# Kernel tuning notes

Measured on AMD Instinct MI355X. Metric: run time of the kernel, lower is better.

Reference implementation:

```python
import jax, jax.numpy as jnp
import numpy as np

DIM = 256
HEADS = 8
DIM_HEAD = 64
INNER = HEADS * DIM_HEAD  # 512
B, N = 4, 1024


def setup_inputs() -> dict:
    key = jax.random.key(0)
    ks = jax.random.split(key, 7)
    x = jax.random.normal(ks[0], (B, N, DIM), dtype=jnp.float32)
    attn_bias = jax.random.normal(ks[1], (B, HEADS, N, N), dtype=jnp.float32)
    s = 1.0 / np.sqrt(DIM)
    Wq = jax.random.normal(ks[2], (DIM, INNER), dtype=jnp.float32) * s
    Wkv = jax.random.normal(ks[3], (DIM, 2 * INNER), dtype=jnp.float32) * s
    # to_out initialized to zero in the torch module; use small random so output is non-trivial
    Wo = jax.random.normal(ks[4], (INNER, DIM), dtype=jnp.float32) * (1.0 / np.sqrt(INNER))
    bo = jnp.zeros((DIM,), dtype=jnp.float32)
    # gating initialized weight=0, bias=1 -> sigmoid(1); use small random weight + bias 1
    Wg = jax.random.normal(ks[5], (DIM, INNER), dtype=jnp.float32) * 0.02
    bg = jnp.ones((INNER,), dtype=jnp.float32)
    return {"x": x, "attn_bias": attn_bias, "Wq": Wq, "Wkv": Wkv,
            "Wo": Wo, "bo": bo, "Wg": Wg, "bg": bg}


def reference(x, attn_bias, Wq, Wkv, Wo, bo, Wg, bg):
    b, n, _ = x.shape
    scale = DIM_HEAD ** -0.5
    q = x @ Wq                                    # [b, n, inner]
    kv = x @ Wkv                                  # [b, n, 2*inner]
    k, v = jnp.split(kv, 2, axis=-1)
    def split_heads(t):
        return t.reshape(b, n, HEADS, DIM_HEAD).transpose(0, 2, 1, 3)  # [b,h,n,d]
    q, k, v = split_heads(q) * scale, split_heads(k), split_heads(v)
    dots = jnp.einsum('bhid,bhjd->bhij', q, k) + attn_bias
    # explicit max-subtract then softmax (matches original; numerically identical)
    attn = jax.nn.softmax(dots, axis=-1)
    out = jnp.einsum('bhij,bhjd->bhid', attn, v)  # [b,h,n,d]
    out = out.transpose(0, 2, 1, 3).reshape(b, n, INNER)
    gates = jax.nn.sigmoid(x @ Wg + bg)
    out = out * gates
    return out @ Wo + bo
```

## Files before the change

### kernel.cpp

```cpp
#include <hip/hip_runtime.h>

typedef unsigned short u16;
typedef unsigned int u32;
typedef __attribute__((ext_vector_type(8))) __bf16 bf16x8;
typedef __attribute__((ext_vector_type(4))) float floatx4;
typedef const __attribute__((address_space(1))) unsigned char glob_u8;
typedef __attribute__((address_space(3))) unsigned char lds_u8;

#define DEV __device__ __forceinline__

DEV u16 f2bf(float f) {
  u32 u = __builtin_bit_cast(u32, f);
  u = (u + 0x7fffu + ((u >> 16) & 1u)) >> 16;
  return (u16)u;
}
DEV float bf2f(u16 h) {
  u32 u = ((u32)h) << 16;
  return __builtin_bit_cast(float, u);
}
DEV floatx4 MFMA(bf16x8 a, bf16x8 b, floatx4 c) {
  return __builtin_amdgcn_mfma_f32_16x16x32_bf16(a, b, c, 0, 0, 0);
}

__global__ void convert_k(const float* __restrict__ x, const float* __restrict__ Wq,
                          const float* __restrict__ Wkv, const float* __restrict__ Wg,
                          const float* __restrict__ Wo,
                          u16* __restrict__ xb, u16* __restrict__ WcatT, u16* __restrict__ WoT) {
  int i = blockIdx.x * 256 + threadIdx.x;
  if (i < 1048576) { xb[i] = f2bf(x[i]); return; }
  i -= 1048576;
  if (i < 524288) {
    int n = i >> 8, kk = i & 255;
    float v;
    if (n < 512) v = Wq[kk * 512 + n];
    else if (n < 1536) v = Wkv[kk * 1024 + (n - 512)];
    else v = Wg[kk * 512 + (n - 1536)];
    WcatT[i] = f2bf(v);
    return;
  }
  i -= 524288;
  if (i < 131072) {
    int n = i >> 9, kk = i & 511;
    WoT[i] = f2bf(Wo[kk * 256 + n]);
  }
}

__global__ __launch_bounds__(256, 4) void gemm_qkvg(
    const u16* __restrict__ xb, const u16* __restrict__ WcatT, const float* __restrict__ bg,
    u16* __restrict__ qb, u16* __restrict__ kfrag, u16* __restrict__ vfrag, u16* __restrict__ gb) {
  __shared__ __attribute__((aligned(16))) u16 As[128 * 40];
  __shared__ __attribute__((aligned(16))) u16 Bs[64 * 40];
  const int tid = threadIdx.x;
  const int wave = tid >> 6, lane = tid & 63;
  const int lane15 = lane & 15, quad = lane >> 4;
  const int rm0 = blockIdx.x * 128;
  const int cn0 = blockIdx.y * 64;
  const int wm = (wave & 1) * 64, wn = (wave >> 1) * 32;
  const int rowA = tid >> 1, segA = (tid & 1) * 16;
  const int rowB = tid >> 2, segB = (tid & 3) * 8;
  floatx4 acc[4][2] = {};
  uint4 a0 = *(const uint4*)(xb + (rm0 + rowA) * 256 + segA);
  uint4 a1 = *(const uint4*)(xb + (rm0 + rowA) * 256 + segA + 8);
  uint4 b0 = *(const uint4*)(WcatT + (cn0 + rowB) * 256 + segB);
#pragma unroll 1
  for (int k0 = 0; k0 < 256; k0 += 32) {
    __syncthreads();
    *(uint4*)(As + rowA * 40 + segA) = a0;
    *(uint4*)(As + rowA * 40 + segA + 8) = a1;
    *(uint4*)(Bs + rowB * 40 + segB) = b0;
    __syncthreads();
    if (k0 < 224) {
      a0 = *(const uint4*)(xb + (rm0 + rowA) * 256 + k0 + 32 + segA);
      a1 = *(const uint4*)(xb + (rm0 + rowA) * 256 + k0 + 32 + segA + 8);
      b0 = *(const uint4*)(WcatT + (cn0 + rowB) * 256 + k0 + 32 + segB);
    }
    bf16x8 af[4], bfr[2];
#pragma unroll
    for (int mt = 0; mt < 4; ++mt) af[mt] = *(const bf16x8*)(As + (wm + mt * 16 + lane15) * 40 + quad * 8);
#pragma unroll
    for (int nt = 0; nt < 2; ++nt) bfr[nt] = *(const bf16x8*)(Bs + (wn + nt * 16 + lane15) * 40 + quad * 8);
#pragma unroll
    for (int mt = 0; mt < 4; ++mt)
#pragma unroll
      for (int nt = 0; nt < 2; ++nt)
        acc[mt][nt] = MFMA(af[mt], bfr[nt], acc[mt][nt]);
  }
#pragma unroll
  for (int mt = 0; mt < 4; ++mt)
#pragma unroll
    for (int nt = 0; nt < 2; ++nt)
#pragma unroll
      for (int r = 0; r < 4; ++r) {
        int row = rm0 + wm + mt * 16 + quad * 4 + r;
        int col = cn0 + wn + nt * 16 + lane15;
        float v = acc[mt][nt][r];
        int b = row >> 10, n = row & 1023;
        if (col < 512) {
          int h = col >> 6, d = col & 63;
          qb[((b * 8 + h) * 1024 + n) * 64 + d] = f2bf(v * 0.125f);
        } else if (col < 1024) {
          int c = col - 512, h = c >> 6, d = c & 63;
          int bh2 = b * 8 + h;
          int t = n >> 4, l15 = n & 15;
          int half = d >> 5, qd = (d >> 3) & 3, e = d & 7;
          kfrag[(size_t)bh2 * 65536 + t * 1024 + half * 512 + (qd * 16 + l15) * 8 + e] = f2bf(v);
        } else if (col < 1536) {
          int c = col - 1024, h = c >> 6, d = c & 63;
          int bh2 = b * 8 + h;
          int t64 = n >> 6, ck = (n >> 5) & 1, qd = (n >> 3) & 3, e = n & 7;
          int dt = d >> 4, l15 = d & 15;
          vfrag[(size_t)bh2 * 65536 + t64 * 4096 + dt * 1024 + ck * 512 + (qd * 16 + l15) * 8 + e] = f2bf(v);
        } else {
          int c = col - 1536;
          float g = 1.0f / (1.0f + __expf(-(v + bg[c])));
          gb[row * 512 + c] = f2bf(g);
        }
      }
}

__global__ __launch_bounds__(256, 3) void attn_part_k(
    const u16* __restrict__ qb, const u16* __restrict__ kfrag, const u16* __restrict__ vfrag,
    const float* __restrict__ bias,
    float* __restrict__ po, float* __restrict__ pl) {
  __shared__ __attribute__((aligned(16))) u16 Kt[4096];
  __shared__ __attribute__((aligned(16))) u16 Vt[4096];
  __shared__ __attribute__((aligned(16))) float Bt[4096];
  __shared__ __attribute__((aligned(16))) u16 Ps[4 * 16 * 72];
  const int tid = threadIdx.x;
  const int wave = tid >> 6, lane = tid & 63;
  const int lane15 = lane & 15, quad = lane >> 4;
  const int bh = blockIdx.x;
  const int q0 = blockIdx.y * 64;
  const int kc = blockIdx.z;

  bf16x8 qf0, qf1;
  {
    const u16* qrow = qb + ((size_t)(bh * 1024 + q0 + wave * 16 + lane15)) * 64 + quad * 8;
    qf0 = *(const bf16x8*)(qrow);
    qf1 = *(const bf16x8*)(qrow + 32);
  }
  bf16x8 ones;
#pragma unroll
  for (int e = 0; e < 8; ++e) ones[e] = __builtin_bit_cast(__bf16, (u16)0x3F80);

  floatx4 oacc[4] = {};
  floatx4 lacc = {};

  u16* Pw = Ps + wave * (16 * 72);
  const u16* kp = kfrag + (size_t)bh * 65536;
  const u16* vp = vfrag + (size_t)bh * 65536;

#pragma unroll 1
  for (int kt = 0; kt < 8; ++kt) {
    const int kb0 = kc * 512 + kt * 64;
    const u16* kS = kp + kb0 * 64;
    const u16* vS = vp + kb0 * 64;
#pragma unroll
    for (int c = 0; c < 2; ++c) {
      int ch = wave * 2 + c;
      __builtin_amdgcn_global_load_lds((glob_u8*)(kS + ch * 512 + lane * 8),
                                       (lds_u8*)(Kt + ch * 512), 16, 0, 0);
      __builtin_amdgcn_global_load_lds((glob_u8*)(vS + ch * 512 + lane * 8),
                                       (lds_u8*)(Vt + ch * 512), 16, 0, 0);
    }
#pragma unroll
    for (int c = 0; c < 4; ++c) {
      int ch = wave * 4 + c;
      const float* bS = bias + ((size_t)(bh * 1024 + q0 + ch * 4 + (lane >> 4))) * 1024 + kb0 + (lane & 15) * 4;
      __builtin_amdgcn_global_load_lds((glob_u8*)bS, (lds_u8*)(Bt + ch * 256), 16, 0, 0);
    }
    __syncthreads();

    floatx4 s[4];
#pragma unroll
    for (int j = 0; j < 4; ++j) {
      bf16x8 kf0 = *(const bf16x8*)(Kt + j * 1024 + lane * 8);
      bf16x8 kf1 = *(const bf16x8*)(Kt + j * 1024 + 512 + lane * 8);
      floatx4 z = {};
      z = MFMA(qf0, kf0, z);
      s[j] = MFMA(qf1, kf1, z);
    }
#pragma unroll
    for (int j = 0; j < 4; ++j)
#pragma unroll
      for (int r = 0; r < 4; ++r)
        s[j][r] = __expf(s[j][r] + Bt[(wave * 16 + quad * 4 + r) * 64 + j * 16 + lane15] - 8.0f);
#pragma unroll
    for (int j = 0; j < 4; ++j)
#pragma unroll
      for (int r = 0; r < 4; ++r)
        Pw[(quad * 4 + r) * 72 + j * 16 + lane15] = f2bf(s[j][r]);
    bf16x8 pf0 = *(const bf16x8*)(Pw + lane15 * 72 + quad * 8);
    bf16x8 pf1 = *(const bf16x8*)(Pw + lane15 * 72 + 32 + quad * 8);

    lacc = MFMA(pf0, ones, lacc);
    lacc = MFMA(pf1, ones, lacc);
#pragma unroll
    for (int dt = 0; dt < 4; ++dt) {
      bf16x8 vf0 = *(const bf16x8*)(Vt + dt * 1024 + lane * 8);
      bf16x8 vf1 = *(const bf16x8*)(Vt + dt * 1024 + 512 + lane * 8);
      oacc[dt] = MFMA(pf0, vf0, oacc[dt]);
      oacc[dt] = MFMA(pf1, vf1, oacc[dt]);
    }
    __syncthreads();
  }

  float* poW = po + ((size_t)(kc * 32 + bh)) * 65536;
#pragma unroll
  for (int dt = 0; dt < 4; ++dt)
#pragma unroll
    for (int r = 0; r < 4; ++r) {
      int qrow = q0 + wave * 16 + quad * 4 + r;
      poW[(size_t)qrow * 64 + dt * 16 + lane15] = oacc[dt][r];
    }
  if (lane15 == 0) {
#pragma unroll
    for (int r = 0; r < 4; ++r) {
      int qrow = q0 + wave * 16 + quad * 4 + r;
      pl[kc * 32768 + bh * 1024 + qrow] = lacc[r];
    }
  }
}

__global__ __launch_bounds__(256) void attn_merge_k(
    const float* __restrict__ po, const float* __restrict__ pl,
    const u16* __restrict__ gb, u16* __restrict__ ogb) {
  int t = blockIdx.x * 256 + threadIdx.x;
  int row = t >> 4;
  int dseg = (t & 15) * 4;
  float inv = 1.0f / (pl[row] + pl[32768 + row]);
  float4 o0 = *(const float4*)(po + (size_t)row * 64 + dseg);
  float4 o1 = *(const float4*)(po + ((size_t)(32768 + row)) * 64 + dseg);
  int bh = row >> 10, q = row & 1023;
  int h = bh & 7, b = bh >> 3;
  size_t gi = ((size_t)(b * 1024 + q)) * 512 + h * 64 + dseg;
  u16 g4[4];
  *(uint2*)g4 = *(const uint2*)(gb + gi);
  u16 r4[4];
  r4[0] = f2bf((o0.x + o1.x) * inv * bf2f(g4[0]));
  r4[1] = f2bf((o0.y + o1.y) * inv * bf2f(g4[1]));
  r4[2] = f2bf((o0.z + o1.z) * inv * bf2f(g4[2]));
  r4[3] = f2bf((o0.w + o1.w) * inv * bf2f(g4[3]));
  *(uint2*)(ogb + gi) = *(uint2*)r4;
}

__global__ __launch_bounds__(256, 4) void gemm_out_part(
    const u16* __restrict__ og, const u16* __restrict__ WoT, float* __restrict__ pout) {
  __shared__ __attribute__((aligned(16))) u16 As[128 * 40];
  __shared__ __attribute__((aligned(16))) u16 Bs[64 * 40];
  const int tid = threadIdx.x;
  const int wave = tid >> 6, lane = tid & 63;
  const int lane15 = lane & 15, quad = lane >> 4;
  const int rm0 = blockIdx.x * 128;
  const int cn0 = blockIdx.y * 64;
  const int kc = blockIdx.z;
  const int wm = (wave & 1) * 64, wn = (wave >> 1) * 32;
  const int rowA = tid >> 1, segA = (tid & 1) * 16;
  const int rowB = tid >> 2, segB = (tid & 3) * 8;
  floatx4 acc[4][2] = {};
  uint4 a0 = *(const uint4*)(og + (rm0 + rowA) * 512 + kc * 128 + segA);
  uint4 a1 = *(const uint4*)(og + (rm0 + rowA) * 512 + kc * 128 + segA + 8);
  uint4 b0 = *(const uint4*)(WoT + (cn0 + rowB) * 512 + kc * 128 + segB);
#pragma unroll 1
  for (int s = 0; s < 4; ++s) {
    const int k0 = kc * 128 + s * 32;
    __syncthreads();
    *(uint4*)(As + rowA * 40 + segA) = a0;
    *(uint4*)(As + rowA * 40 + segA + 8) = a1;
    *(uint4*)(Bs + rowB * 40 + segB) = b0;
    __syncthreads();
    if (s < 3) {
      a0 = *(const uint4*)(og + (rm0 + rowA) * 512 + k0 + 32 + segA);
      a1 = *(const uint4*)(og + (rm0 + rowA) * 512 + k0 + 32 + segA + 8);
      b0 = *(const uint4*)(WoT + (cn0 + rowB) * 512 + k0 + 32 + segB);
    }
    bf16x8 af[4], bfr[2];
#pragma unroll
    for (int mt = 0; mt < 4; ++mt) af[mt] = *(const bf16x8*)(As + (wm + mt * 16 + lane15) * 40 + quad * 8);
#pragma unroll
    for (int nt = 0; nt < 2; ++nt) bfr[nt] = *(const bf16x8*)(Bs + (wn + nt * 16 + lane15) * 40 + quad * 8);
#pragma unroll
    for (int mt = 0; mt < 4; ++mt)
#pragma unroll
      for (int nt = 0; nt < 2; ++nt)
        acc[mt][nt] = MFMA(af[mt], bfr[nt], acc[mt][nt]);
  }
  float* pw = pout + (size_t)kc * 1048576;
#pragma unroll
  for (int mt = 0; mt < 4; ++mt)
#pragma unroll
    for (int nt = 0; nt < 2; ++nt)
#pragma unroll
      for (int r = 0; r < 4; ++r) {
        int row = rm0 + wm + mt * 16 + quad * 4 + r;
        int col = cn0 + wn + nt * 16 + lane15;
        pw[(size_t)row * 256 + col] = acc[mt][nt][r];
      }
}

__global__ __launch_bounds__(256) void reduce4_bo(
    const float* __restrict__ pout, const float* __restrict__ bo, float* __restrict__ out) {
  int g = blockIdx.x * 256 + threadIdx.x;
  const float4* p = (const float4*)pout;
  float4 s0 = p[g], s1 = p[g + 262144], s2 = p[g + 524288], s3 = p[g + 786432];
  int col = (g * 4) & 255;
  float4 bb = *(const float4*)(bo + col);
  float4 r;
  r.x = s0.x + s1.x + s2.x + s3.x + bb.x;
  r.y = s0.y + s1.y + s2.y + s3.y + bb.y;
  r.z = s0.z + s1.z + s2.z + s3.z + bb.z;
  r.w = s0.w + s1.w + s2.w + s3.w + bb.w;
  ((float4*)out)[g] = r;
}

extern "C" void kernel_launch(void* const* d_in, const int* in_sizes, int n_in,
                              void* d_out, int out_size, void* d_ws, size_t ws_size,
                              hipStream_t stream) {
  const float* x = (const float*)d_in[0];
  const float* bias = (const float*)d_in[1];
  const float* Wq = (const float*)d_in[2];
  const float* Wkv = (const float*)d_in[3];
  const float* Wo = (const float*)d_in[4];
  const float* bo = (const float*)d_in[5];
  const float* Wg = (const float*)d_in[6];
  const float* bg = (const float*)d_in[7];
  float* out = (float*)d_out;
  char* ws = (char*)d_ws;
  u16* xb    = (u16*)(ws);
  u16* WcatT = (u16*)(ws + 2097152);
  u16* WoT   = (u16*)(ws + 3145728);
  u16* qb    = (u16*)(ws + 3407872);
  u16* kfrag = (u16*)(ws + 7602176);
  u16* vfrag = (u16*)(ws + 11796480);
  u16* gb    = (u16*)(ws + 15990784);
  u16* ogb   = (u16*)(ws + 20185088);
  float* po  = (float*)(ws + 24379392);
  float* pl  = (float*)(ws);
  float* pout = po;

  convert_k<<<6656, 256, 0, stream>>>(x, Wq, Wkv, Wg, Wo, xb, WcatT, WoT);
  dim3 g1(32, 32);
  gemm_qkvg<<<g1, 256, 0, stream>>>(xb, WcatT, bg, qb, kfrag, vfrag, gb);
  dim3 g2(32, 16, 2);
  attn_part_k<<<g2, 256, 0, stream>>>(qb, kfrag, vfrag, bias, po, pl);
  attn_merge_k<<<2048, 256, 0, stream>>>(po, pl, gb, ogb);
  dim3 g3(32, 4, 4);
  gemm_out_part<<<g3, 256, 0, stream>>>(ogb, WoT, pout);
  reduce4_bo<<<1024, 256, 0, stream>>>(pout, bo, out);
}
```

Baseline: 264.5 us.

## Remove split-K in attention and output GEMM, fusing merge and reduce steps

Attention now runs each query block over all 1024 keys in a single block with double-buffered LDS staging of K, V and bias tiles, and applies normalization and gating directly in the epilogue. This drops the partial-output buffers and the separate merge kernel. The output GEMM also drops split-K and adds the bias in its epilogue, which removes the reduce kernel. The trade-off is fewer blocks and therefore less parallelism (512 attention blocks instead of 1024), plus lower occupancy from the doubled LDS footprint.

```diff
diff --git a/kernel.cpp b/kernel.cpp
--- a/kernel.cpp
+++ b/kernel.cpp
@@ -118,20 +118,18 @@
       }
 }
 
-__global__ __launch_bounds__(256, 3) void attn_part_k(
+__global__ __launch_bounds__(256, 2) void attn_k(
     const u16* __restrict__ qb, const u16* __restrict__ kfrag, const u16* __restrict__ vfrag,
-    const float* __restrict__ bias,
-    float* __restrict__ po, float* __restrict__ pl) {
-  __shared__ __attribute__((aligned(16))) u16 Kt[4096];
-  __shared__ __attribute__((aligned(16))) u16 Vt[4096];
-  __shared__ __attribute__((aligned(16))) float Bt[4096];
+    const float* __restrict__ bias, const u16* __restrict__ gb, u16* __restrict__ ogb) {
+  __shared__ __attribute__((aligned(16))) u16 Kt[2][4096];
+  __shared__ __attribute__((aligned(16))) u16 Vt[2][4096];
+  __shared__ __attribute__((aligned(16))) float Bt[2][4096];
   __shared__ __attribute__((aligned(16))) u16 Ps[4 * 16 * 72];
   const int tid = threadIdx.x;
   const int wave = tid >> 6, lane = tid & 63;
   const int lane15 = lane & 15, quad = lane >> 4;
   const int bh = blockIdx.x;
   const int q0 = blockIdx.y * 64;
-  const int kc = blockIdx.z;
 
   bf16x8 qf0, qf1;
   {
@@ -150,32 +148,40 @@
   const u16* kp = kfrag + (size_t)bh * 65536;
   const u16* vp = vfrag + (size_t)bh * 65536;
 
-#pragma unroll 1
-  for (int kt = 0; kt < 8; ++kt) {
-    const int kb0 = kc * 512 + kt * 64;
+  auto stage = [&](int kt, int bufi) {
+    const int kb0 = kt * 64;
     const u16* kS = kp + kb0 * 64;
     const u16* vS = vp + kb0 * 64;
 #pragma unroll
     for (int c = 0; c < 2; ++c) {
       int ch = wave * 2 + c;
       __builtin_amdgcn_global_load_lds((glob_u8*)(kS + ch * 512 + lane * 8),
-                                       (lds_u8*)(Kt + ch * 512), 16, 0, 0);
+                                       (lds_u8*)(&Kt[bufi][ch * 512]), 16, 0, 0);
       __builtin_amdgcn_global_load_lds((glob_u8*)(vS + ch * 512 + lane * 8),
-                                       (lds_u8*)(Vt + ch * 512), 16, 0, 0);
+                                       (lds_u8*)(&Vt[bufi][ch * 512]), 16, 0, 0);
     }
 #pragma unroll
     for (int c = 0; c < 4; ++c) {
       int ch = wave * 4 + c;
-      const float* bS = bias + ((size_t)(bh * 1024 + q0 + ch * 4 + (lane >> 4))) * 1024 + kb0 + (lane & 15) * 4;
-      __builtin_amdgcn_global_load_lds((glob_u8*)bS, (lds_u8*)(Bt + ch * 256), 16, 0, 0);
-    }
-    __syncthreads();
-
+      const float* bS = bias + ((size_t)(bh * 1024 + q0 + ch * 4 + quad)) * 1024 + kb0 + lane15 * 4;
+      __builtin_amdgcn_global_load_lds((glob_u8*)bS, (lds_u8*)(&Bt[bufi][ch * 256]), 16, 0, 0);
+    }
+  };
+
+  stage(0, 0);
+  __syncthreads();
+  int cur = 0;
+#pragma unroll 1
+  for (int kt = 0; kt < 16; ++kt) {
+    if (kt < 15) stage(kt + 1, cur ^ 1);
+    const u16* Ktc = Kt[cur];
+    const u16* Vtc = Vt[cur];
+    const float* Btc = Bt[cur];
     floatx4 s[4];
 #pragma unroll
     for (int j = 0; j < 4; ++j) {
-      bf16x8 kf0 = *(const bf16x8*)(Kt + j * 1024 + lane * 8);
-      bf16x8 kf1 = *(const bf16x8*)(Kt + j * 1024 + 512 + lane * 8);
+      bf16x8 kf0 = *(const bf16x8*)(Ktc + j * 1024 + lane * 8);
+      bf16x8 kf1 = *(const bf16x8*)(Ktc + j * 1024 + 512 + lane * 8);
       floatx4 z = {};
       z = MFMA(qf0, kf0, z);
       s[j] = MFMA(qf1, kf1, z);
@@ -184,7 +190,7 @@
     for (int j = 0; j < 4; ++j)
 #pragma unroll
       for (int r = 0; r < 4; ++r)
-        s[j][r] = __expf(s[j][r] + Bt[(wave * 16 + quad * 4 + r) * 64 + j * 16 + lane15] - 8.0f);
+        s[j][r] = __expf(s[j][r] + Btc[(wave * 16 + quad * 4 + r) * 64 + j * 16 + lane15] - 8.0f);
 #pragma unroll
     for (int j = 0; j < 4; ++j)
 #pragma unroll
@@ -197,120 +203,77 @@
     lacc = MFMA(pf1, ones, lacc);
 #pragma unroll
     for (int dt = 0; dt < 4; ++dt) {
-      bf16x8 vf0 = *(const bf16x8*)(Vt + dt * 1024 + lane * 8);
-      bf16x8 vf1 = *(const bf16x8*)(Vt + dt * 1024 + 512 + lane * 8);
+      bf16x8 vf0 = *(const bf16x8*)(Vtc + dt * 1024 + lane * 8);
+      bf16x8 vf1 = *(const bf16x8*)(Vtc + dt * 1024 + 512 + lane * 8);
       oacc[dt] = MFMA(pf0, vf0, oacc[dt]);
       oacc[dt] = MFMA(pf1, vf1, oacc[dt]);
     }
     __syncthreads();
-  }
-
-  float* poW = po + ((size_t)(kc * 32 + bh)) * 65536;
-#pragma unroll
-  for (int dt = 0; dt < 4; ++dt)
-#pragma unroll
-    for (int r = 0; r < 4; ++r) {
-      int qrow = q0 + wave * 16 + quad * 4 + r;
-      poW[(size_t)qrow * 64 + dt * 16 + lane15] = oacc[dt][r];
-    }
-  if (lane15 == 0) {
-#pragma unroll
-    for (int r = 0; r < 4; ++r) {
-      int qrow = q0 + wave * 16 + quad * 4 + r;
-      pl[kc * 32768 + bh * 1024 + qrow] = lacc[r];
-    }
-  }
-}
-
-__global__ __launch_bounds__(256) void attn_merge_k(
-    const float* __restrict__ po, const float* __restrict__ pl,
-    const u16* __restrict__ gb, u16* __restrict__ ogb) {
-  int t = blockIdx.x * 256 + threadIdx.x;
-  int row = t >> 4;
-  int dseg = (t & 15) * 4;
-  float inv = 1.0f / (pl[row] + pl[32768 + row]);
-  float4 o0 = *(const float4*)(po + (size_t)row * 64 + dseg);
-  float4 o1 = *(const float4*)(po + ((size_t)(32768 + row)) * 64 + dseg);
-  int bh = row >> 10, q = row & 1023;
-  int h = bh & 7, b = bh >> 3;
-  size_t gi = ((size_t)(b * 1024 + q)) * 512 + h * 64 + dseg;
-  u16 g4[4];
-  *(uint2*)g4 = *(const uint2*)(gb + gi);
-  u16 r4[4];
-  r4[0] = f2bf((o0.x + o1.x) * inv * bf2f(g4[0]));
-  r4[1] = f2bf((o0.y + o1.y) * inv * bf2f(g4[1]));
-  r4[2] = f2bf((o0.z + o1.z) * inv * bf2f(g4[2]));
-  r4[3] = f2bf((o0.w + o1.w) * inv * bf2f(g4[3]));
-  *(uint2*)(ogb + gi) = *(uint2*)r4;
-}
-
-__global__ __launch_bounds__(256, 4) void gemm_out_part(
-    const u16* __restrict__ og, const u16* __restrict__ WoT, float* __restrict__ pout) {
-  __shared__ __attribute__((aligned(16))) u16 As[128 * 40];
+    cur ^= 1;
+  }
+
+  const int b = bh >> 3, h = bh & 7;
+#pragma unroll
+  for (int r = 0; r < 4; ++r) {
+    int q = q0 + wave * 16 + quad * 4 + r;
+    float inv = 1.0f / lacc[r];
+    size_t base = ((size_t)(b * 1024 + q)) * 512 + h * 64;
+#pragma unroll
+    for (int dt = 0; dt < 4; ++dt) {
+      size_t gi = base + dt * 16 + lane15;
+      ogb[gi] = f2bf(oacc[dt][r] * inv * bf2f(gb[gi]));
+    }
+  }
+}
+
+__global__ __launch_bounds__(256, 4) void gemm_out_k(
+    const u16* __restrict__ og, const u16* __restrict__ WoT,
+    const float* __restrict__ bo, float* __restrict__ out) {
+  __shared__ __attribute__((aligned(16))) u16 As[64 * 40];
   __shared__ __attribute__((aligned(16))) u16 Bs[64 * 40];
   const int tid = threadIdx.x;
   const int wave = tid >> 6, lane = tid & 63;
   const int lane15 = lane & 15, quad = lane >> 4;
-  const int rm0 = blockIdx.x * 128;
+  const int rm0 = blockIdx.x * 64;
   const int cn0 = blockIdx.y * 64;
-  const int kc = blockIdx.z;
-  const int wm = (wave & 1) * 64, wn = (wave >> 1) * 32;
-  const int rowA = tid >> 1, segA = (tid & 1) * 16;
-  const int rowB = tid >> 2, segB = (tid & 3) * 8;
-  floatx4 acc[4][2] = {};
-  uint4 a0 = *(const uint4*)(og + (rm0 + rowA) * 512 + kc * 128 + segA);
-  uint4 a1 = *(const uint4*)(og + (rm0 + rowA) * 512 + kc * 128 + segA + 8);
-  uint4 b0 = *(const uint4*)(WoT + (cn0 + rowB) * 512 + kc * 128 + segB);
+  const int wm = (wave & 1) * 32, wn = (wave >> 1) * 32;
+  const int rowA = tid >> 2, segA = (tid & 3) * 8;
+  floatx4 acc[2][2] = {};
+  uint4 a0 = *(const uint4*)(og + (rm0 + rowA) * 512 + segA);
+  uint4 b0 = *(const uint4*)(WoT + (cn0 + rowA) * 512 + segA);
 #pragma unroll 1
-  for (int s = 0; s < 4; ++s) {
-    const int k0 = kc * 128 + s * 32;
+  for (int k0 = 0; k0 < 512; k0 += 32) {
     __syncthreads();
     *(uint4*)(As + rowA * 40 + segA) = a0;
-    *(uint4*)(As + rowA * 40 + segA + 8) = a1;
-    *(uint4*)(Bs + rowB * 40 + segB) = b0;
-    __syncthreads();
-    if (s < 3) {
+    *(uint4*)(Bs + rowA * 40 + segA) = b0;
+    __syncthreads();
+    if (k0 < 480) {
       a0 = *(const uint4*)(og + (rm0 + rowA) * 512 + k0 + 32 + segA);
-      a1 = *(const uint4*)(og + (rm0 + rowA) * 512 + k0 + 32 + segA + 8);
-      b0 = *(const uint4*)(WoT + (cn0 + rowB) * 512 + k0 + 32 + segB);
-    }
-    bf16x8 af[4], bfr[2];
-#pragma unroll
-    for (int mt = 0; mt < 4; ++mt) af[mt] = *(const bf16x8*)(As + (wm + mt * 16 + lane15) * 40 + quad * 8);
+      b0 = *(const uint4*)(WoT + (cn0 + rowA) * 512 + k0 + 32 + segA);
+    }
+    bf16x8 af[2], bfr[2];
+#pragma unroll
+    for (int mt = 0; mt < 2; ++mt) af[mt] = *(const bf16x8*)(As + (wm + mt * 16 + lane15) * 40 + quad * 8);
 #pragma unroll
     for (int nt = 0; nt < 2; ++nt) bfr[nt] = *(const bf16x8*)(Bs + (wn + nt * 16 + lane15) * 40 + quad * 8);
 #pragma unroll
-    for (int mt = 0; mt < 4; ++mt)
+    for (int mt = 0; mt < 2; ++mt)
 #pragma unroll
       for (int nt = 0; nt < 2; ++nt)
         acc[mt][nt] = MFMA(af[mt], bfr[nt], acc[mt][nt]);
   }
-  float* pw = pout + (size_t)kc * 1048576;
-#pragma unroll
-  for (int mt = 0; mt < 4; ++mt)
-#pragma unroll
-    for (int nt = 0; nt < 2; ++nt)
+#pragma unroll
+  for (int nt = 0; nt < 2; ++nt) {
+    int col = cn0 + wn + nt * 16 + lane15;
+    float bv = bo[col];
+#pragma unroll
+    for (int mt = 0; mt < 2; ++mt)
 #pragma unroll
       for (int r = 0; r < 4; ++r) {
         int row = rm0 + wm + mt * 16 + quad * 4 + r;
-        int col = cn0 + wn + nt * 16 + lane15;
-        pw[(size_t)row * 256 + col] = acc[mt][nt][r];
+        out[(size_t)row * 256 + col] = acc[mt][nt][r] + bv;
       }
-}
-
-__global__ __launch_bounds__(256) void reduce4_bo(
-    const float* __restrict__ pout, const float* __restrict__ bo, float* __restrict__ out) {
-  int g = blockIdx.x * 256 + threadIdx.x;
-  const float4* p = (const float4*)pout;
-  float4 s0 = p[g], s1 = p[g + 262144], s2 = p[g + 524288], s3 = p[g + 786432];
-  int col = (g * 4) & 255;
-  float4 bb = *(const float4*)(bo + col);
-  float4 r;
-  r.x = s0.x + s1.x + s2.x + s3.x + bb.x;
-  r.y = s0.y + s1.y + s2.y + s3.y + bb.y;
-  r.z = s0.z + s1.z + s2.z + s3.z + bb.z;
-  r.w = s0.w + s1.w + s2.w + s3.w + bb.w;
-  ((float4*)out)[g] = r;
+  }
 }
 
 extern "C" void kernel_launch(void* const* d_in, const int* in_sizes, int n_in,
@@ -334,17 +297,12 @@
   u16* vfrag = (u16*)(ws + 11796480);
   u16* gb    = (u16*)(ws + 15990784);
   u16* ogb   = (u16*)(ws + 20185088);
-  float* po  = (float*)(ws + 24379392);
-  float* pl  = (float*)(ws);
-  float* pout = po;
 
   convert_k<<<6656, 256, 0, stream>>>(x, Wq, Wkv, Wg, Wo, xb, WcatT, WoT);
   dim3 g1(32, 32);
   gemm_qkvg<<<g1, 256, 0, stream>>>(xb, WcatT, bg, qb, kfrag, vfrag, gb);
-  dim3 g2(32, 16, 2);
-  attn_part_k<<<g2, 256, 0, stream>>>(qb, kfrag, vfrag, bias, po, pl);
-  attn_merge_k<<<2048, 256, 0, stream>>>(po, pl, gb, ogb);
-  dim3 g3(32, 4, 4);
-  gemm_out_part<<<g3, 256, 0, stream>>>(ogb, WoT, pout);
-  reduce4_bo<<<1024, 256, 0, stream>>>(pout, bo, out);
-}
+  dim3 g2(32, 16);
+  attn_k<<<g2, 256, 0, stream>>>(qb, kfrag, vfrag, bias, gb, ogb);
+  dim3 g3(64, 4);
+  gemm_out_k<<<g3, 256, 0, stream>>>(ogb, WoT, bo, out);
+}
```

After: 252.6 us. 1.05x faster.
